# Kernel tuning notes

Measured on AMD Instinct MI355X. Metric: run time of the kernel, lower is better.

Reference implementation:

```python
import jax, jax.numpy as jnp
import numpy as np


def setup_inputs() -> dict:
    key = jax.random.key(0)
    ks = jax.random.split(key, 6)
    B, T, C, H, E = 4, 2048, 768, 3072, 16
    scale = 0.02
    return {
        "x": jax.random.normal(ks[0], (B, T, C), dtype=jnp.float32),
        "w_shared_fc": jax.random.normal(ks[1], (C, 2 * H), dtype=jnp.float32) * scale,
        "w_shared_proj": jax.random.normal(ks[2], (H, C), dtype=jnp.float32) * scale,
        "w_experts_fc": jax.random.normal(ks[3], (E, C, 2 * H), dtype=jnp.float32) * scale,
        "w_experts_proj": jax.random.normal(ks[4], (E, H, C), dtype=jnp.float32) * scale,
        "w_gate": jax.random.normal(ks[5], (C, E), dtype=jnp.float32) * scale,
        "expert_bias": jnp.zeros((E,), dtype=jnp.float32),
        "top_k": 4,
    }


def _swiglu(h):
    gate, val = jnp.split(h, 2, axis=-1)
    return jax.nn.silu(gate) * val


def reference(x, w_shared_fc, w_shared_proj, w_experts_fc, w_experts_proj,
              w_gate, expert_bias, top_k):
    B, T, C = x.shape
    E = expert_bias.shape[0]
    N = B * T

    # shared expert (applied to every token)
    shared = _swiglu(x @ w_shared_fc) @ w_shared_proj  # [B,T,C]

    # top-k sigmoid routing
    gate_logits = x @ w_gate + expert_bias            # [B,T,E]
    gate_w = jax.nn.sigmoid(gate_logits)
    top_w, top_idx = jax.lax.top_k(gate_w, top_k)     # [B,T,K]
    top_w = top_w / jnp.sum(top_w, axis=-1, keepdims=True)

    # dense per-token/per-expert weight matrix [N,E] (zero for unrouted)
    w_dense = jnp.sum(jax.nn.one_hot(top_idx, E, dtype=x.dtype) * top_w[..., None],
                      axis=-2).reshape(N, E)

    flat_x = x.reshape(N, C)

    def body(acc, params):
        wfc, wproj, we = params  # [C,2H], [H,C], [N]
        out = _swiglu(flat_x @ wfc) @ wproj  # [N,C]
        return acc + we[:, None] * out, None

    routed, _ = jax.lax.scan(body, jnp.zeros_like(flat_x),
                             (w_experts_fc, w_experts_proj, w_dense.T))
    return shared + routed.reshape(B, T, C)
```

## Files before the change

### kernel.cpp

```cpp
#include <hip/hip_runtime.h>
#include <hip/hip_bf16.h>

typedef __hip_bfloat16 bf16;
typedef __attribute__((ext_vector_type(8))) short short8;
typedef __attribute__((ext_vector_type(4))) float float4v;

#define BK 32

__device__ __forceinline__ void gload16(const bf16* g, bf16* s) {
    __builtin_amdgcn_global_load_lds(
        (const __attribute__((address_space(1))) void*)g,
        (__attribute__((address_space(3))) void*)s, 16, 0, 0);
}

#define BAR() do { asm volatile("" ::: "memory"); __builtin_amdgcn_s_barrier(); asm volatile("" ::: "memory"); } while (0)


__global__ void k_convert_x(const float* __restrict__ in, bf16* __restrict__ out,
                            int n, int* __restrict__ cnt) {
    if (blockIdx.x == 0 && threadIdx.x < 16) cnt[threadIdx.x] = 0;
    int i = (blockIdx.x * blockDim.x + threadIdx.x) * 4;
    if (i + 3 < n) {
        float4 v = *(const float4*)(in + i);
        out[i + 0] = __float2bfloat16(v.x);
        out[i + 1] = __float2bfloat16(v.y);
        out[i + 2] = __float2bfloat16(v.z);
        out[i + 3] = __float2bfloat16(v.w);
    }
}

__global__ __launch_bounds__(256) void k_transpose64(
    const float* __restrict__ in, bf16* __restrict__ out, int R, int S, int fuse) {
    __shared__ float tile[64][65];
    size_t mat = (size_t)blockIdx.z * R * S;
    int s0 = blockIdx.x * 64, r0 = blockIdx.y * 64;
    int tid = threadIdx.x;
    int rr = tid >> 4, sc = (tid & 15) * 4;
    #pragma unroll
    for (int i = 0; i < 4; ++i) {
        float4 v = *(const float4*)(in + mat + (size_t)(r0 + rr + i * 16) * S + s0 + sc);
        tile[rr + i * 16][sc + 0] = v.x;
        tile[rr + i * 16][sc + 1] = v.y;
        tile[rr + i * 16][sc + 2] = v.z;
        tile[rr + i * 16][sc + 3] = v.w;
    }
    __syncthreads();
    int ss = tid >> 3, rc = (tid & 7) * 8;
    #pragma unroll
    for (int i = 0; i < 2; ++i) {
        int sl = ss + i * 32;
        int sg = s0 + sl;
        int so = sg;
        if (fuse) {
            int half = (sg >= 3072) ? 1 : 0;
            int idx = sg - half * 3072;
            so = ((idx >> 4) << 5) | (half << 4) | (idx & 15);
        }
        bf16 tmp[8];
        #pragma unroll
        for (int j = 0; j < 8; ++j) tmp[j] = __float2bfloat16(tile[rc + j][sl]);
        *(uint4*)(out + mat + (size_t)so * R + r0 + rc) = *(uint4*)tmp;
    }
}

__global__ void k_gate(const float* __restrict__ x, const float* __restrict__ wg,
                       const float* __restrict__ bias, int* __restrict__ cnt,
                       int* __restrict__ tok, float* __restrict__ wl,
                       int* __restrict__ slotk) {
    __shared__ float gates[16][17];
    int t = threadIdx.x;
    int tl = t >> 4;
    int e = t & 15;
    int token = blockIdx.x * 16 + tl;
    const float* xr = x + (size_t)token * 768;
    float acc = 0.f;
    #pragma unroll 4
    for (int c = 0; c < 768; ++c) acc += xr[c] * wg[c * 16 + e];
    acc += bias[e];
    gates[tl][e] = 1.f / (1.f + expf(-acc));
    __syncthreads();
    if (t < 16) {
        int token2 = blockIdx.x * 16 + t;
        float g[16];
        #pragma unroll
        for (int j = 0; j < 16; ++j) g[j] = gates[t][j];
        int idx[4]; float w[4]; float sum = 0.f;
        #pragma unroll
        for (int k = 0; k < 4; ++k) {
            float best = -1e30f; int bi = 0;
            #pragma unroll
            for (int j = 0; j < 16; ++j)
                if (g[j] > best) { best = g[j]; bi = j; }
            idx[k] = bi; w[k] = best; sum += best; g[bi] = -1e30f;
        }
        float inv = 1.f / sum;
        for (int k = 0; k < 4; ++k) {
            int slot = atomicAdd(&cnt[idx[k]], 1);
            tok[(idx[k] << 13) + slot] = token2;
            wl[(idx[k] << 13) + slot] = w[k] * inv;
            slotk[token2 * 4 + k] = (idx[k] << 13) | slot;
        }
    }
}

__global__ void k_offsets(const int* __restrict__ cnt, int* __restrict__ offs) {
    if (threadIdx.x == 0) {
        int s = 0;
        for (int e = 0; e < 16; ++e) { offs[e] = s; s += cnt[e]; }
    }
}

__global__ __launch_bounds__(192) void k_combine(
    const float* __restrict__ routed, const int* __restrict__ slotk,
    const int* __restrict__ offs, float* __restrict__ out) {
    int t = blockIdx.x;
    int c4 = threadIdx.x * 4;
    float* op = out + (size_t)t * 768 + c4;
    float4 acc = *(float4*)op;
    #pragma unroll
    for (int k = 0; k < 4; ++k) {
        int sk = slotk[t * 4 + k];
        int e = sk >> 13, sl = sk & 8191;
        const float* row = routed + (size_t)(offs[e] + sl) * 768 + c4;
        float4 v = *(const float4*)row;
        acc.x += v.x; acc.y += v.y; acc.z += v.z; acc.w += v.w;
    }
    *(float4*)op = acc;
}

template<int GATHER>
__device__ __forceinline__ void fc8_body(
    const bf16* __restrict__ A, const bf16* __restrict__ BT,
    bf16* __restrict__ act, const int* __restrict__ cnt,
    const int* __restrict__ offs, const int* __restrict__ tok)
{
    const int Kd = 768, H = 3072;
    int e = blockIdx.z;
    int m0 = blockIdx.y * 256;
    int n0 = blockIdx.x * 256;
    int M; size_t actbase = 0; const int* tl = nullptr;
    if (GATHER) {
        M = cnt[e];
        if (m0 >= M) return;
        tl = tok + (e << 13);
        actbase = (size_t)offs[e] * H;
        BT += (size_t)e * 6144 * Kd;
    } else {
        M = 8192;
    }

    __shared__ bf16 lds[65536];

    int tid = threadIdx.x;
    int lane = tid & 63;
    int w = tid >> 6;
    int wm = w & 1, wn = w >> 1;
    int quad = lane >> 4, l16 = lane & 15;

    int srow = tid >> 3;
    int g0 = (tid & 7) ^ (srow & 7);

    const bf16* gA[2][2]; const bf16* gB[2][2];
    #pragma unroll
    for (int h = 0; h < 2; ++h) {
        int ra = m0 + h * 128 + srow;
        int rb = n0 + h * 128 + srow;
        int a0 = GATHER ? tl[min(ra, M - 1)] : ra;
        int a1 = GATHER ? tl[min(ra + 64, M - 1)] : (ra + 64);
        gA[h][0] = A + (size_t)a0 * Kd + g0 * 8;
        gA[h][1] = A + (size_t)a1 * Kd + g0 * 8;
        gB[h][0] = BT + (size_t)rb * Kd + g0 * 8;
        gB[h][1] = BT + (size_t)(rb + 64) * Kd + g0 * 8;
    }

    auto stageA = [&](int buf, int kt) {
        bf16* d = lds + buf * 32768;
        gload16(gA[0][0] + kt * 64, d + tid * 8);
        gload16(gA[0][1] + kt * 64, d + (tid + 512) * 8);
        gload16(gA[1][0] + kt * 64, d + 8192 + tid * 8);
        gload16(gA[1][1] + kt * 64, d + 8192 + (tid + 512) * 8);
    };
    auto stageB = [&](int buf, int kt) {
        bf16* d = lds + buf * 32768 + 16384;
        gload16(gB[0][0] + kt * 64, d + tid * 8);
        gload16(gB[0][1] + kt * 64, d + (tid + 512) * 8);
        gload16(gB[1][0] + kt * 64, d + 8192 + tid * 8);
        gload16(gB[1][1] + kt * 64, d + 8192 + (tid + 512) * 8);
    };

    int swz0 = ((quad    ) ^ (l16 & 7)) * 8;
    int swz1 = ((quad | 4) ^ (l16 & 7)) * 8;
    int aBase = wm * 8192 + l16 * 64;
    int bBase = 16384 + wn * 4096 + l16 * 64;

    float4v acc[8][4] = {};

    stageA(0, 0);
    stageB(0, 0);
    asm volatile("s_waitcnt vmcnt(0)" ::: "memory");
    BAR();

    for (int t = 0; t < 12; ++t) {
        const bf16* cb = lds + (t & 1) * 32768;
        int nb = (t & 1) ^ 1;
        bool pf = (t < 11);
        short8 ar[4], br[4];

        #pragma unroll
        for (int nf = 0; nf < 4; ++nf)
            br[nf] = *(const short8*)(cb + bBase + nf * 1024 + swz0);
        #pragma unroll
        for (int mf = 0; mf < 4; ++mf)
            ar[mf] = *(const short8*)(cb + aBase + mf * 1024 + swz0);
        if (pf) stageA(nb, t + 1);
        __builtin_amdgcn_s_setprio(1);
        #pragma unroll
        for (int mf = 0; mf < 4; ++mf)
            #pragma unroll
            for (int nf = 0; nf < 4; ++nf)
                acc[mf][nf] = __builtin_amdgcn_mfma_f32_16x16x32_bf16(ar[mf], br[nf], acc[mf][nf], 0, 0, 0);
        __builtin_amdgcn_s_setprio(0);
        BAR();

        #pragma unroll
        for (int mf = 0; mf < 4; ++mf)
            ar[mf] = *(const short8*)(cb + aBase + (mf + 4) * 1024 + swz0);
        if (pf) stageB(nb, t + 1);
        __builtin_amdgcn_s_setprio(1);
        #pragma unroll
        for (int mf = 0; mf < 4; ++mf)
            #pragma unroll
            for (int nf = 0; nf < 4; ++nf)
                acc[mf + 4][nf] = __builtin_amdgcn_mfma_f32_16x16x32_bf16(ar[mf], br[nf], acc[mf + 4][nf], 0, 0, 0);
        __builtin_amdgcn_s_setprio(0);
        asm volatile("s_waitcnt vmcnt(4)" ::: "memory");
        BAR();

        #pragma unroll
        for (int nf = 0; nf < 4; ++nf)
            br[nf] = *(const short8*)(cb + bBase + nf * 1024 + swz1);
        #pragma unroll
        for (int mf = 0; mf < 4; ++mf)
            ar[mf] = *(const short8*)(cb + aBase + mf * 1024 + swz1);
        __builtin_amdgcn_s_setprio(1);
        #pragma unroll
        for (int mf = 0; mf < 4; ++mf)
            #pragma unroll
            for (int nf = 0; nf < 4; ++nf)
                acc[mf][nf] = __builtin_amdgcn_mfma_f32_16x16x32_bf16(ar[mf], br[nf], acc[mf][nf], 0, 0, 0);
        __builtin_amdgcn_s_setprio(0);
        BAR();

        #pragma unroll
        for (int mf = 0; mf < 4; ++mf)
            ar[mf] = *(const short8*)(cb + aBase + (mf + 4) * 1024 + swz1);
        __builtin_amdgcn_s_setprio(1);
        #pragma unroll
        for (int mf = 0; mf < 4; ++mf)
            #pragma unroll
            for (int nf = 0; nf < 4; ++nf)
                acc[mf + 4][nf] = __builtin_amdgcn_mfma_f32_16x16x32_bf16(ar[mf], br[nf], acc[mf + 4][nf], 0, 0, 0);
        __builtin_amdgcn_s_setprio(0);
        asm volatile("s_waitcnt vmcnt(0)" ::: "memory");
        BAR();
    }

    int orow = m0 + wm * 128;
    int ocol = (n0 + wn * 64) >> 1;
    #pragma unroll
    for (int mf = 0; mf < 8; ++mf)
        #pragma unroll
        for (int j = 0; j < 2; ++j)
            #pragma unroll
            for (int r = 0; r < 4; ++r) {
                int mrow = orow + mf * 16 + quad * 4 + r;
                if (GATHER && mrow >= M) continue;
                int col = ocol + j * 16 + l16;
                float g = acc[mf][2 * j][r];
                float v = acc[mf][2 * j + 1][r];
                float sg = g / (1.f + __expf(-g));
                act[actbase + (size_t)mrow * H + col] = __float2bfloat16(sg * v);
            }
}

__global__ __launch_bounds__(512) void k_fc_shared(
    const bf16* __restrict__ A, const bf16* __restrict__ BT, bf16* __restrict__ act,
    const int* __restrict__ cnt, const int* __restrict__ offs, const int* __restrict__ tok) {
    fc8_body<0>(A, BT, act, cnt, offs, tok);
}
__global__ __launch_bounds__(512) void k_fc_routed(
    const bf16* __restrict__ A, const bf16* __restrict__ BT, bf16* __restrict__ act,
    const int* __restrict__ cnt, const int* __restrict__ offs, const int* __restrict__ tok) {
    fc8_body<1>(A, BT, act, cnt, offs, tok);
}

template<int ROUTED>
__device__ __forceinline__ void proj_body(
    const bf16* __restrict__ Aact, const bf16* __restrict__ PT,
    float* __restrict__ out, const int* __restrict__ cnt,
    const int* __restrict__ offs, const float* __restrict__ wl) {
    const int Kd = 3072;
    int e = blockIdx.z;
    int m0 = blockIdx.y * 256;
    int n0 = blockIdx.x * 128;
    int M;
    size_t abase = 0;
    int roffs = 0;
    if (ROUTED) {
        M = cnt[e];
        if (m0 >= M) return;
        roffs = offs[e];
        abase = (size_t)roffs * Kd;
        PT += (size_t)e * 768 * Kd;
    } else {
        M = 8192;
    }

    __shared__ bf16 sA[256 * BK];
    __shared__ bf16 sB[128 * BK];

    int tid = threadIdx.x, lane = tid & 63, w = tid >> 6;
    int wm = w & 3, wn = w >> 2;

    int srA0 = tid >> 2;
    int srA1 = (tid + 512) >> 2;
    int k2A0 = (tid & 3) ^ ((srA0 >> 1) & 3);
    int k2A1 = (tid & 3) ^ ((srA1 >> 1) & 3);
    int srB = tid >> 2;
    int k2B = (tid & 3) ^ ((srB >> 1) & 3);

    int ra0 = min(m0 + srA0, M - 1);
    int ra1 = min(m0 + srA1, M - 1);
    const bf16* gA0 = Aact + abase + (size_t)ra0 * Kd + k2A0 * 8;
    const bf16* gA1 = Aact + abase + (size_t)ra1 * Kd + k2A1 * 8;
    const bf16* gB  = PT + (size_t)(n0 + srB) * Kd + k2B * 8;
    bf16* sA0p = sA + tid * 8;
    bf16* sA1p = sA + (tid + 512) * 8;
    bf16* sBp  = sB + tid * 8;

    float4v acc[4][4] = {};
    int quad = lane >> 4, l16 = lane & 15;
    int q2 = quad ^ ((l16 >> 1) & 3);

    for (int kk = 0; kk < Kd; kk += BK) {
        __syncthreads();
        gload16(gA0 + kk, sA0p);
        gload16(gA1 + kk, sA1p);
        gload16(gB + kk, sBp);
        __syncthreads();
        short8 af[4], bb[4];
        #pragma unroll
        for (int i = 0; i < 4; ++i) {
            int rowa = wm * 64 + i * 16 + l16;
            int rowb = wn * 64 + i * 16 + l16;
            af[i] = *(const short8*)(sA + rowa * BK + q2 * 8);
            bb[i] = *(const short8*)(sB + rowb * BK + q2 * 8);
        }
        #pragma unroll
        for (int mf = 0; mf < 4; ++mf)
            #pragma unroll
            for (int nf = 0; nf < 4; ++nf)
                acc[mf][nf] = __builtin_amdgcn_mfma_f32_16x16x32_bf16(af[mf], bb[nf], acc[mf][nf], 0, 0, 0);
    }

    #pragma unroll
    for (int mf = 0; mf < 4; ++mf) {
        #pragma unroll
        for (int r = 0; r < 4; ++r) {
            int mr = m0 + wm * 64 + mf * 16 + quad * 4 + r;
            if (ROUTED) {
                if (mr < M) {
                    float wgt = wl[(e << 13) + mr];
                    float* orow = out + (size_t)(roffs + mr) * 768;
                    #pragma unroll
                    for (int nf = 0; nf < 4; ++nf) {
                        int col = n0 + wn * 64 + nf * 16 + l16;
                        orow[col] = wgt * acc[mf][nf][r];
                    }
                }
            } else {
                #pragma unroll
                for (int nf = 0; nf < 4; ++nf) {
                    int col = n0 + wn * 64 + nf * 16 + l16;
                    out[(size_t)mr * 768 + col] = acc[mf][nf][r];
                }
            }
        }
    }
}

__global__ __launch_bounds__(512) void k_proj_shared(
    const bf16* __restrict__ Aact, const bf16* __restrict__ PT, float* __restrict__ out,
    const int* __restrict__ cnt, const int* __restrict__ offs, const float* __restrict__ wl) {
    proj_body<0>(Aact, PT, out, cnt, offs, wl);
}
__global__ __launch_bounds__(512) void k_proj_routed(
    const bf16* __restrict__ Aact, const bf16* __restrict__ PT, float* __restrict__ out,
    const int* __restrict__ cnt, const int* __restrict__ offs, const float* __restrict__ wl) {
    proj_body<1>(Aact, PT, out, cnt, offs, wl);
}


extern "C" void kernel_launch(void* const* d_in, const int* in_sizes, int n_in,
                              void* d_out, int out_size, void* d_ws, size_t ws_size,
                              hipStream_t stream) {
    const float* x    = (const float*)d_in[0];
    const float* wfc  = (const float*)d_in[1];
    const float* wpr  = (const float*)d_in[2];
    const float* wefc = (const float*)d_in[3];
    const float* wepr = (const float*)d_in[4];
    const float* wg   = (const float*)d_in[5];
    const float* eb   = (const float*)d_in[6];
    float* out = (float*)d_out;

    char* p = (char*)d_ws;
    bf16* x_bf  = (bf16*)p; p += (size_t)8192 * 768 * 2;
    bf16* fcT_s = (bf16*)p; p += (size_t)6144 * 768 * 2;
    bf16* prT_s = (bf16*)p; p += (size_t)768 * 3072 * 2;
    bf16* fcT_e = (bf16*)p; p += (size_t)16 * 6144 * 768 * 2;
    bf16* prT_e = (bf16*)p; p += (size_t)16 * 768 * 3072 * 2;
    bf16* act_s = (bf16*)p; p += (size_t)8192 * 3072 * 2;
    bf16* act_r = (bf16*)p; p += (size_t)32768 * 3072 * 2;
    int* cnt    = (int*)p;  p += 64;
    int* offs   = (int*)p;  p += 64;
    int* tok    = (int*)p;  p += (size_t)16 * 8192 * 4;
    float* wl   = (float*)p; p += (size_t)16 * 8192 * 4;
    int* slotk  = (int*)p;  p += (size_t)8192 * 4 * 4;
    float* routed_out = (float*)fcT_e;

    k_convert_x<<<dim3(6144), dim3(256), 0, stream>>>(x, x_bf, 8192 * 768, cnt);
    k_transpose64<<<dim3(96, 12, 1), dim3(256), 0, stream>>>(wfc, fcT_s, 768, 6144, 1);
    k_transpose64<<<dim3(12, 48, 1), dim3(256), 0, stream>>>(wpr, prT_s, 3072, 768, 0);
    k_transpose64<<<dim3(96, 12, 16), dim3(256), 0, stream>>>(wefc, fcT_e, 768, 6144, 1);
    k_transpose64<<<dim3(12, 48, 16), dim3(256), 0, stream>>>(wepr, prT_e, 3072, 768, 0);
    k_gate<<<dim3(512), dim3(256), 0, stream>>>(x, wg, eb, cnt, tok, wl, slotk);
    k_offsets<<<dim3(1), dim3(64), 0, stream>>>(cnt, offs);

    k_fc_shared<<<dim3(24, 32, 1), dim3(512), 0, stream>>>(x_bf, fcT_s, act_s, cnt, offs, tok);
    k_fc_routed<<<dim3(24, 32, 16), dim3(512), 0, stream>>>(x_bf, fcT_e, act_r, cnt, offs, tok);
    k_proj_shared<<<dim3(6, 32, 1), dim3(512), 0, stream>>>(act_s, prT_s, out, cnt, offs, wl);
    k_proj_routed<<<dim3(6, 32, 16), dim3(512), 0, stream>>>(act_r, prT_e, routed_out, cnt, offs, wl);
    k_combine<<<dim3(8192), dim3(192), 0, stream>>>(routed_out, slotk, offs, out);
}
```

Measured before the change: 1.597 ms.

## Unify shared and routed GEMMs into single launches with shared 256x256 double-buffered core

```diff
diff --git a/kernel.cpp b/kernel.cpp
--- a/kernel.cpp
+++ b/kernel.cpp
@@ -4,8 +4,6 @@
 typedef __hip_bfloat16 bf16;
 typedef __attribute__((ext_vector_type(8))) short short8;
 typedef __attribute__((ext_vector_type(4))) float float4v;
-
-#define BK 32
 
 __device__ __forceinline__ void gload16(const bf16* g, bf16* s) {
     __builtin_amdgcn_global_load_lds(
@@ -128,91 +126,48 @@
     *(float4*)op = acc;
 }
 
-template<int GATHER>
-__device__ __forceinline__ void fc8_body(
-    const bf16* __restrict__ A, const bf16* __restrict__ BT,
-    bf16* __restrict__ act, const int* __restrict__ cnt,
-    const int* __restrict__ offs, const int* __restrict__ tok)
+template<int KD>
+__device__ __forceinline__ void gemm_core(
+    const bf16* const* gA, const bf16* const* gB,
+    bf16* lds, int tid, float4v (&acc)[8][4])
 {
-    const int Kd = 768, H = 3072;
-    int e = blockIdx.z;
-    int m0 = blockIdx.y * 256;
-    int n0 = blockIdx.x * 256;
-    int M; size_t actbase = 0; const int* tl = nullptr;
-    if (GATHER) {
-        M = cnt[e];
-        if (m0 >= M) return;
-        tl = tok + (e << 13);
-        actbase = (size_t)offs[e] * H;
-        BT += (size_t)e * 6144 * Kd;
-    } else {
-        M = 8192;
-    }
-
-    __shared__ bf16 lds[65536];
-
-    int tid = threadIdx.x;
+    constexpr int NT = KD / 64;
     int lane = tid & 63;
-    int w = tid >> 6;
-    int wm = w & 1, wn = w >> 1;
+    int w = tid >> 6, wm = w & 1, wn = w >> 1;
     int quad = lane >> 4, l16 = lane & 15;
-
-    int srow = tid >> 3;
-    int g0 = (tid & 7) ^ (srow & 7);
-
-    const bf16* gA[2][2]; const bf16* gB[2][2];
-    #pragma unroll
-    for (int h = 0; h < 2; ++h) {
-        int ra = m0 + h * 128 + srow;
-        int rb = n0 + h * 128 + srow;
-        int a0 = GATHER ? tl[min(ra, M - 1)] : ra;
-        int a1 = GATHER ? tl[min(ra + 64, M - 1)] : (ra + 64);
-        gA[h][0] = A + (size_t)a0 * Kd + g0 * 8;
-        gA[h][1] = A + (size_t)a1 * Kd + g0 * 8;
-        gB[h][0] = BT + (size_t)rb * Kd + g0 * 8;
-        gB[h][1] = BT + (size_t)(rb + 64) * Kd + g0 * 8;
-    }
-
-    auto stageA = [&](int buf, int kt) {
-        bf16* d = lds + buf * 32768;
-        gload16(gA[0][0] + kt * 64, d + tid * 8);
-        gload16(gA[0][1] + kt * 64, d + (tid + 512) * 8);
-        gload16(gA[1][0] + kt * 64, d + 8192 + tid * 8);
-        gload16(gA[1][1] + kt * 64, d + 8192 + (tid + 512) * 8);
-    };
-    auto stageB = [&](int buf, int kt) {
-        bf16* d = lds + buf * 32768 + 16384;
-        gload16(gB[0][0] + kt * 64, d + tid * 8);
-        gload16(gB[0][1] + kt * 64, d + (tid + 512) * 8);
-        gload16(gB[1][0] + kt * 64, d + 8192 + tid * 8);
-        gload16(gB[1][1] + kt * 64, d + 8192 + (tid + 512) * 8);
-    };
-
     int swz0 = ((quad    ) ^ (l16 & 7)) * 8;
     int swz1 = ((quad | 4) ^ (l16 & 7)) * 8;
     int aBase = wm * 8192 + l16 * 64;
     int bBase = 16384 + wn * 4096 + l16 * 64;
 
-    float4v acc[8][4] = {};
-
-    stageA(0, 0);
-    stageB(0, 0);
+    auto stage = [&](int buf, int kt) {
+        bf16* dB = lds + buf * 32768 + 16384;
+        gload16(gB[0] + kt * 64, dB + tid * 8);
+        gload16(gB[1] + kt * 64, dB + (tid + 512) * 8);
+        gload16(gB[2] + kt * 64, dB + 8192 + tid * 8);
+        gload16(gB[3] + kt * 64, dB + 8192 + (tid + 512) * 8);
+        bf16* dA = lds + buf * 32768;
+        gload16(gA[0] + kt * 64, dA + tid * 8);
+        gload16(gA[1] + kt * 64, dA + (tid + 512) * 8);
+        gload16(gA[2] + kt * 64, dA + 8192 + tid * 8);
+        gload16(gA[3] + kt * 64, dA + 8192 + (tid + 512) * 8);
+    };
+
+    stage(0, 0);
     asm volatile("s_waitcnt vmcnt(0)" ::: "memory");
     BAR();
 
-    for (int t = 0; t < 12; ++t) {
+    for (int t = 0; t < NT; ++t) {
         const bf16* cb = lds + (t & 1) * 32768;
-        int nb = (t & 1) ^ 1;
-        bool pf = (t < 11);
         short8 ar[4], br[4];
 
+        if (t < NT - 1) stage((t & 1) ^ 1, t + 1);
         #pragma unroll
         for (int nf = 0; nf < 4; ++nf)
             br[nf] = *(const short8*)(cb + bBase + nf * 1024 + swz0);
         #pragma unroll
         for (int mf = 0; mf < 4; ++mf)
             ar[mf] = *(const short8*)(cb + aBase + mf * 1024 + swz0);
-        if (pf) stageA(nb, t + 1);
         __builtin_amdgcn_s_setprio(1);
         #pragma unroll
         for (int mf = 0; mf < 4; ++mf)
@@ -225,7 +180,6 @@
         #pragma unroll
         for (int mf = 0; mf < 4; ++mf)
             ar[mf] = *(const short8*)(cb + aBase + (mf + 4) * 1024 + swz0);
-        if (pf) stageB(nb, t + 1);
         __builtin_amdgcn_s_setprio(1);
         #pragma unroll
         for (int mf = 0; mf < 4; ++mf)
@@ -233,7 +187,6 @@
             for (int nf = 0; nf < 4; ++nf)
                 acc[mf + 4][nf] = __builtin_amdgcn_mfma_f32_16x16x32_bf16(ar[mf], br[nf], acc[mf + 4][nf], 0, 0, 0);
         __builtin_amdgcn_s_setprio(0);
-        asm volatile("s_waitcnt vmcnt(4)" ::: "memory");
         BAR();
 
         #pragma unroll
@@ -264,7 +217,49 @@
         asm volatile("s_waitcnt vmcnt(0)" ::: "memory");
         BAR();
     }
-
+}
+
+__global__ __launch_bounds__(512) void k_fc(
+    const bf16* __restrict__ A, const bf16* __restrict__ fcT, bf16* __restrict__ act,
+    const int* __restrict__ cnt, const int* __restrict__ offs, const int* __restrict__ tok)
+{
+    const int Kd = 768;
+    int e = blockIdx.z;
+    int m0 = blockIdx.x * 256;
+    int n0 = blockIdx.y * 256;
+    int M; size_t actbase; const int* tl = nullptr;
+    if (e == 16) {
+        M = 8192; actbase = (size_t)32768 * 3072;
+    } else {
+        M = cnt[e];
+        if (m0 >= M) return;
+        tl = tok + (e << 13);
+        actbase = (size_t)offs[e] * 3072;
+    }
+    const bf16* BT = fcT + (size_t)e * 6144 * Kd;
+
+    __shared__ bf16 lds[65536];
+    int tid = threadIdx.x;
+    int srow = tid >> 3;
+    int g0 = (tid & 7) ^ (srow & 7);
+
+    const bf16* gA[4]; const bf16* gB[4];
+    #pragma unroll
+    for (int h = 0; h < 2; ++h) {
+        int ra = m0 + h * 128 + srow;
+        int a0 = tl ? tl[min(ra, M - 1)] : ra;
+        int a1 = tl ? tl[min(ra + 64, M - 1)] : (ra + 64);
+        gA[h * 2 + 0] = A + (size_t)a0 * Kd + g0 * 8;
+        gA[h * 2 + 1] = A + (size_t)a1 * Kd + g0 * 8;
+        gB[h * 2 + 0] = BT + (size_t)(n0 + h * 128 + srow) * Kd + g0 * 8;
+        gB[h * 2 + 1] = BT + (size_t)(n0 + h * 128 + srow + 64) * Kd + g0 * 8;
+    }
+
+    float4v acc[8][4] = {};
+    gemm_core<768>(gA, gB, lds, tid, acc);
+
+    int lane = tid & 63, w = tid >> 6, wm = w & 1, wn = w >> 1;
+    int quad = lane >> 4, l16 = lane & 15;
     int orow = m0 + wm * 128;
     int ocol = (n0 + wn * 64) >> 1;
     #pragma unroll
@@ -274,130 +269,79 @@
             #pragma unroll
             for (int r = 0; r < 4; ++r) {
                 int mrow = orow + mf * 16 + quad * 4 + r;
-                if (GATHER && mrow >= M) continue;
+                if (tl && mrow >= M) continue;
                 int col = ocol + j * 16 + l16;
                 float g = acc[mf][2 * j][r];
                 float v = acc[mf][2 * j + 1][r];
                 float sg = g / (1.f + __expf(-g));
-                act[actbase + (size_t)mrow * H + col] = __float2bfloat16(sg * v);
+                act[actbase + (size_t)mrow * 3072 + col] = __float2bfloat16(sg * v);
             }
 }
 
-__global__ __launch_bounds__(512) void k_fc_shared(
-    const bf16* __restrict__ A, const bf16* __restrict__ BT, bf16* __restrict__ act,
-    const int* __restrict__ cnt, const int* __restrict__ offs, const int* __restrict__ tok) {
-    fc8_body<0>(A, BT, act, cnt, offs, tok);
-}
-__global__ __launch_bounds__(512) void k_fc_routed(
-    const bf16* __restrict__ A, const bf16* __restrict__ BT, bf16* __restrict__ act,
-    const int* __restrict__ cnt, const int* __restrict__ offs, const int* __restrict__ tok) {
-    fc8_body<1>(A, BT, act, cnt, offs, tok);
-}
-
-template<int ROUTED>
-__device__ __forceinline__ void proj_body(
-    const bf16* __restrict__ Aact, const bf16* __restrict__ PT,
-    float* __restrict__ out, const int* __restrict__ cnt,
-    const int* __restrict__ offs, const float* __restrict__ wl) {
+__global__ __launch_bounds__(512) void k_proj(
+    const bf16* __restrict__ act, const bf16* __restrict__ prT,
+    float* __restrict__ out, float* __restrict__ routed_out,
+    const int* __restrict__ cnt, const int* __restrict__ offs, const float* __restrict__ wl)
+{
     const int Kd = 3072;
     int e = blockIdx.z;
-    int m0 = blockIdx.y * 256;
-    int n0 = blockIdx.x * 128;
-    int M;
-    size_t abase = 0;
-    int roffs = 0;
-    if (ROUTED) {
+    int m0 = blockIdx.x * 256;
+    int n0 = blockIdx.y * 256;
+    int M; size_t abase; int roffs = 0;
+    bool rt = (e != 16);
+    if (rt) {
         M = cnt[e];
         if (m0 >= M) return;
         roffs = offs[e];
         abase = (size_t)roffs * Kd;
-        PT += (size_t)e * 768 * Kd;
     } else {
-        M = 8192;
-    }
-
-    __shared__ bf16 sA[256 * BK];
-    __shared__ bf16 sB[128 * BK];
-
-    int tid = threadIdx.x, lane = tid & 63, w = tid >> 6;
-    int wm = w & 3, wn = w >> 2;
-
-    int srA0 = tid >> 2;
-    int srA1 = (tid + 512) >> 2;
-    int k2A0 = (tid & 3) ^ ((srA0 >> 1) & 3);
-    int k2A1 = (tid & 3) ^ ((srA1 >> 1) & 3);
-    int srB = tid >> 2;
-    int k2B = (tid & 3) ^ ((srB >> 1) & 3);
-
-    int ra0 = min(m0 + srA0, M - 1);
-    int ra1 = min(m0 + srA1, M - 1);
-    const bf16* gA0 = Aact + abase + (size_t)ra0 * Kd + k2A0 * 8;
-    const bf16* gA1 = Aact + abase + (size_t)ra1 * Kd + k2A1 * 8;
-    const bf16* gB  = PT + (size_t)(n0 + srB) * Kd + k2B * 8;
-    bf16* sA0p = sA + tid * 8;
-    bf16* sA1p = sA + (tid + 512) * 8;
-    bf16* sBp  = sB + tid * 8;
-
-    float4v acc[4][4] = {};
+        M = 8192; abase = (size_t)32768 * Kd;
+    }
+    const bf16* BT = prT + (size_t)e * 768 * Kd;
+
+    __shared__ bf16 lds[65536];
+    int tid = threadIdx.x;
+    int srow = tid >> 3;
+    int g0 = (tid & 7) ^ (srow & 7);
+
+    const bf16* gA[4]; const bf16* gB[4];
+    #pragma unroll
+    for (int h = 0; h < 2; ++h) {
+        int ra = m0 + h * 128 + srow;
+        int a0 = rt ? min(ra, M - 1) : ra;
+        int a1 = rt ? min(ra + 64, M - 1) : (ra + 64);
+        gA[h * 2 + 0] = act + abase + (size_t)a0 * Kd + g0 * 8;
+        gA[h * 2 + 1] = act + abase + (size_t)a1 * Kd + g0 * 8;
+        gB[h * 2 + 0] = BT + (size_t)(n0 + h * 128 + srow) * Kd + g0 * 8;
+        gB[h * 2 + 1] = BT + (size_t)(n0 + h * 128 + srow + 64) * Kd + g0 * 8;
+    }
+
+    float4v acc[8][4] = {};
+    gemm_core<3072>(gA, gB, lds, tid, acc);
+
+    int lane = tid & 63, w = tid >> 6, wm = w & 1, wn = w >> 1;
     int quad = lane >> 4, l16 = lane & 15;
-    int q2 = quad ^ ((l16 >> 1) & 3);
-
-    for (int kk = 0; kk < Kd; kk += BK) {
-        __syncthreads();
-        gload16(gA0 + kk, sA0p);
-        gload16(gA1 + kk, sA1p);
-        gload16(gB + kk, sBp);
-        __syncthreads();
-        short8 af[4], bb[4];
-        #pragma unroll
-        for (int i = 0; i < 4; ++i) {
-            int rowa = wm * 64 + i * 16 + l16;
-            int rowb = wn * 64 + i * 16 + l16;
-            af[i] = *(const short8*)(sA + rowa * BK + q2 * 8);
-            bb[i] = *(const short8*)(sB + rowb * BK + q2 * 8);
-        }
-        #pragma unroll
-        for (int mf = 0; mf < 4; ++mf)
-            #pragma unroll
-            for (int nf = 0; nf < 4; ++nf)
-                acc[mf][nf] = __builtin_amdgcn_mfma_f32_16x16x32_bf16(af[mf], bb[nf], acc[mf][nf], 0, 0, 0);
-    }
-
-    #pragma unroll
-    for (int mf = 0; mf < 4; ++mf) {
+    int orow = m0 + wm * 128;
+    int ocol = n0 + wn * 64;
+    #pragma unroll
+    for (int mf = 0; mf < 8; ++mf)
         #pragma unroll
         for (int r = 0; r < 4; ++r) {
-            int mr = m0 + wm * 64 + mf * 16 + quad * 4 + r;
-            if (ROUTED) {
-                if (mr < M) {
-                    float wgt = wl[(e << 13) + mr];
-                    float* orow = out + (size_t)(roffs + mr) * 768;
-                    #pragma unroll
-                    for (int nf = 0; nf < 4; ++nf) {
-                        int col = n0 + wn * 64 + nf * 16 + l16;
-                        orow[col] = wgt * acc[mf][nf][r];
-                    }
-                }
+            int mr = orow + mf * 16 + quad * 4 + r;
+            if (rt) {
+                if (mr >= M) continue;
+                float wgt = wl[(e << 13) + mr];
+                float* orowp = routed_out + (size_t)(roffs + mr) * 768;
+                #pragma unroll
+                for (int nf = 0; nf < 4; ++nf)
+                    orowp[ocol + nf * 16 + l16] = wgt * acc[mf][nf][r];
             } else {
+                float* orowp = out + (size_t)mr * 768;
                 #pragma unroll
-                for (int nf = 0; nf < 4; ++nf) {
-                    int col = n0 + wn * 64 + nf * 16 + l16;
-                    out[(size_t)mr * 768 + col] = acc[mf][nf][r];
-                }
+                for (int nf = 0; nf < 4; ++nf)
+                    orowp[ocol + nf * 16 + l16] = acc[mf][nf][r];
             }
         }
-    }
-}
-
-__global__ __launch_bounds__(512) void k_proj_shared(
-    const bf16* __restrict__ Aact, const bf16* __restrict__ PT, float* __restrict__ out,
-    const int* __restrict__ cnt, const int* __restrict__ offs, const float* __restrict__ wl) {
-    proj_body<0>(Aact, PT, out, cnt, offs, wl);
-}
-__global__ __launch_bounds__(512) void k_proj_routed(
-    const bf16* __restrict__ Aact, const bf16* __restrict__ PT, float* __restrict__ out,
-    const int* __restrict__ cnt, const int* __restrict__ offs, const float* __restrict__ wl) {
-    proj_body<1>(Aact, PT, out, cnt, offs, wl);
 }
 
 
@@ -415,30 +359,25 @@
 
     char* p = (char*)d_ws;
     bf16* x_bf  = (bf16*)p; p += (size_t)8192 * 768 * 2;
-    bf16* fcT_s = (bf16*)p; p += (size_t)6144 * 768 * 2;
-    bf16* prT_s = (bf16*)p; p += (size_t)768 * 3072 * 2;
-    bf16* fcT_e = (bf16*)p; p += (size_t)16 * 6144 * 768 * 2;
-    bf16* prT_e = (bf16*)p; p += (size_t)16 * 768 * 3072 * 2;
-    bf16* act_s = (bf16*)p; p += (size_t)8192 * 3072 * 2;
-    bf16* act_r = (bf16*)p; p += (size_t)32768 * 3072 * 2;
+    bf16* fcT   = (bf16*)p; p += (size_t)17 * 6144 * 768 * 2;
+    bf16* prT   = (bf16*)p; p += (size_t)17 * 768 * 3072 * 2;
+    bf16* act   = (bf16*)p; p += (size_t)40960 * 3072 * 2;
     int* cnt    = (int*)p;  p += 64;
     int* offs   = (int*)p;  p += 64;
     int* tok    = (int*)p;  p += (size_t)16 * 8192 * 4;
     float* wl   = (float*)p; p += (size_t)16 * 8192 * 4;
     int* slotk  = (int*)p;  p += (size_t)8192 * 4 * 4;
-    float* routed_out = (float*)fcT_e;
+    float* routed_out = (float*)fcT;
 
     k_convert_x<<<dim3(6144), dim3(256), 0, stream>>>(x, x_bf, 8192 * 768, cnt);
-    k_transpose64<<<dim3(96, 12, 1), dim3(256), 0, stream>>>(wfc, fcT_s, 768, 6144, 1);
-    k_transpose64<<<dim3(12, 48, 1), dim3(256), 0, stream>>>(wpr, prT_s, 3072, 768, 0);
-    k_transpose64<<<dim3(96, 12, 16), dim3(256), 0, stream>>>(wefc, fcT_e, 768, 6144, 1);
-    k_transpose64<<<dim3(12, 48, 16), dim3(256), 0, stream>>>(wepr, prT_e, 3072, 768, 0);
+    k_transpose64<<<dim3(96, 12, 16), dim3(256), 0, stream>>>(wefc, fcT, 768, 6144, 1);
+    k_transpose64<<<dim3(96, 12, 1), dim3(256), 0, stream>>>(wfc, fcT + (size_t)16 * 6144 * 768, 768, 6144, 1);
+    k_transpose64<<<dim3(12, 48, 16), dim3(256), 0, stream>>>(wepr, prT, 3072, 768, 0);
+    k_transpose64<<<dim3(12, 48, 1), dim3(256), 0, stream>>>(wpr, prT + (size_t)16 * 768 * 3072, 3072, 768, 0);
     k_gate<<<dim3(512), dim3(256), 0, stream>>>(x, wg, eb, cnt, tok, wl, slotk);
     k_offsets<<<dim3(1), dim3(64), 0, stream>>>(cnt, offs);
 
-    k_fc_shared<<<dim3(24, 32, 1), dim3(512), 0, stream>>>(x_bf, fcT_s, act_s, cnt, offs, tok);
-    k_fc_routed<<<dim3(24, 32, 16), dim3(512), 0, stream>>>(x_bf, fcT_e, act_r, cnt, offs, tok);
-    k_proj_shared<<<dim3(6, 32, 1), dim3(512), 0, stream>>>(act_s, prT_s, out, cnt, offs, wl);
-    k_proj_routed<<<dim3(6, 32, 16), dim3(512), 0, stream>>>(act_r, prT_e, routed_out, cnt, offs, wl);
+    k_fc<<<dim3(32, 24, 17), dim3(512), 0, stream>>>(x_bf, fcT, act, cnt, offs, tok);
+    k_proj<<<dim3(32, 3, 17), dim3(512), 0, stream>>>(act, prT, out, routed_out, cnt, offs, wl);
     k_combine<<<dim3(8192), dim3(192), 0, stream>>>(routed_out, slotk, offs, out);
 }
```

Result: slower. 2.887 ms (+80.9%).
